# Kernel tuning notes

Hardware: AMD Instinct MI355X
Metric: run time of the kernel (lower is better)

## Reference

```python
import jax, jax.numpy as jnp
import numpy as np

MODEL_DIM = 256
NUM_HEAD = 8
HEAD_DIM = MODEL_DIM // NUM_HEAD  # 32
ROT_DIM_AXIS = int(0.5 * HEAD_DIM)  # 16 per axis, 32 total rotated channels
LN_EPS = 1e-5
MASK_BIAS = -1e9  # fp32 precision
SCALE = HEAD_DIM ** -0.5
INIT_RANGE = 0.02
N_LAYERS = 6


def _rotate_half(x):
    # interleaved pairs: (d r) with r=2 -> (-x2, x1) re-interleaved
    x = x.reshape(*x.shape[:-1], -1, 2)
    x1, x2 = x[..., 0], x[..., 1]
    return jnp.stack([-x2, x1], axis=-1).reshape(*x.shape[:-2], -1)


def _axial_freqs(seqlen):
    # RotaryEmbedding('lang' freqs) over t = linspace(-1, 1, seqlen)
    inv_freq = 1.0 / (10000.0 ** (jnp.arange(0, ROT_DIM_AXIS, 2, dtype=jnp.float32) / ROT_DIM_AXIS))
    t = jnp.linspace(-1.0, 1.0, seqlen, dtype=jnp.float32)
    f = jnp.repeat(t[:, None] * inv_freq[None, :], 2, axis=-1)  # (s, ROT_DIM_AXIS)
    fh = jnp.broadcast_to(f[:, None, :], (seqlen, seqlen, ROT_DIM_AXIS))
    fw = jnp.broadcast_to(f[None, :, :], (seqlen, seqlen, ROT_DIM_AXIS))
    return jnp.concatenate([fh, fw], axis=-1)  # (s, s, 2*ROT_DIM_AXIS)


def _apply_rotary(freqs, t):
    rot_dim = freqs.shape[-1]
    t_rot, t_pass = t[..., :rot_dim], t[..., rot_dim:]
    t_rot = t_rot * jnp.cos(freqs) + _rotate_half(t_rot) * jnp.sin(freqs)
    return jnp.concatenate([t_rot, t_pass], axis=-1)


def setup_inputs() -> dict:
    key = jax.random.key(0)
    k1, k2, k3, k4 = jax.random.split(key, 4)
    b, s = 2, 128
    pair_act = jax.random.normal(k1, (b, s, s, MODEL_DIM), dtype=jnp.float32)
    pair_mask = jax.random.randint(k2, (b, s, s), 0, 2).astype(bool)  # True = masked
    Wqkv = jax.random.normal(k3, (3 * MODEL_DIM, MODEL_DIM), dtype=jnp.float32) * INIT_RANGE
    Wout = jax.random.normal(k4, (MODEL_DIM, MODEL_DIM), dtype=jnp.float32) * (INIT_RANGE / np.sqrt(2 * N_LAYERS))
    ln_gamma = jnp.ones((MODEL_DIM,), dtype=jnp.float32)
    ln_beta = jnp.zeros((MODEL_DIM,), dtype=jnp.float32)
    return {"pair_act": pair_act, "pair_mask": pair_mask, "ln_gamma": ln_gamma,
            "ln_beta": ln_beta, "Wqkv": Wqkv, "Wout": Wout}


def reference(pair_act, pair_mask, ln_gamma, ln_beta, Wqkv, Wout):
    # orientation == 'per_row': no axis swap
    b, s = pair_act.shape[0], pair_act.shape[1]
    # LayerNorm over model_dim
    mu = jnp.mean(pair_act, axis=-1, keepdims=True)
    var = jnp.var(pair_act, axis=-1, keepdims=True)
    x = (pair_act - mu) * jax.lax.rsqrt(var + LN_EPS) * ln_gamma + ln_beta
    # QKV projection (no bias)
    qkv = jnp.einsum('bxyd,ed->bxye', x, Wqkv)  # (b, s, s, 3*MODEL_DIM)
    q, k, v = jnp.split(qkv, 3, axis=-1)
    # 2D axial rotary on first 2*ROT_DIM_AXIS channels of the feature dim
    freqs = _axial_freqs(s)  # (s, s, 32)
    q = _apply_rotary(freqs, q)
    k = _apply_rotary(freqs, k)
    # multihead attention per row (axis s1 independent)
    q = q.reshape(b, s, s, NUM_HEAD, HEAD_DIM)
    k = k.reshape(b, s, s, NUM_HEAD, HEAD_DIM)
    v = v.reshape(b, s, s, NUM_HEAD, HEAD_DIM)
    scores = jnp.einsum('bxqhd,bxkhd->bxhqk', q, k) * SCALE  # (b, s1, h, s2, s2)
    mask = pair_mask[:, :, None, None, :]  # (b, s1, 1, 1, s2)
    scores = jnp.where(mask, MASK_BIAS, scores)
    attn = jax.nn.softmax(scores, axis=-1)
    out = jnp.einsum('bxhqk,bxkhd->bxqhd', attn, v).reshape(b, s, s, MODEL_DIM)
    return jnp.einsum('bxyd,ed->bxye', out, Wout)
```

## Files before the change

### kernel.cpp

```cpp
#include <hip/hip_runtime.h>
#include <math.h>
#include <stdint.h>

typedef __attribute__((ext_vector_type(8))) short short8;
typedef __attribute__((ext_vector_type(4))) float floatx4;

#define LN_EPS 1e-5f
#define ATT_SCALE 0.17677669529663687f

__device__ __constant__ float INVF[8] = {
    1.0f, 0.31622776601683794f, 0.1f, 0.031622776601683794f,
    0.01f, 0.0031622776601683794f, 0.001f, 0.00031622776601683794f};

__device__ inline unsigned short f2bf(float f) {
    unsigned u = __float_as_uint(f);
    u += 0x7fffu + ((u >> 16) & 1u);
    return (unsigned short)(u >> 16);
}

__device__ inline void gl_lds16(const unsigned short* g, unsigned short* l) {
    __builtin_amdgcn_global_load_lds(
        (const __attribute__((address_space(1))) void*)(uintptr_t)g,
        (__attribute__((address_space(3))) void*)(uintptr_t)l, 16, 0, 0);
}

__device__ inline void stage_tile(const unsigned short* __restrict__ Wsrc,
                                  unsigned short* dst, int w, int lane) {
    #pragma unroll
    for (int i = 0; i < 4; ++i) {
        int rbase = i * 16 + w * 2;
        int row = rbase + (lane >> 5);
        int sl = lane & 31;
        int c = (sl & ~7) | ((sl & 7) ^ (row & 7));
        gl_lds16(Wsrc + (size_t)row * 256 + c * 8, dst + rbase * 256);
    }
}

#define VM0() asm volatile("s_waitcnt vmcnt(0)" ::: "memory")
#define LG0() asm volatile("s_waitcnt lgkmcnt(0)" ::: "memory")
#define SBAR()                                 \
    do {                                       \
        __builtin_amdgcn_s_barrier();          \
        __builtin_amdgcn_sched_barrier(0);     \
    } while (0)

__global__ __launch_bounds__(256)
void prep_w(const float* __restrict__ wq, const float* __restrict__ wo,
            unsigned short* __restrict__ bq, unsigned short* __restrict__ bo) {
    int g = blockIdx.x * 256 + threadIdx.x;
    const float* src;
    unsigned short* dst;
    if (g < 49152) { src = wq + (size_t)g * 4; dst = bq + (size_t)g * 4; }
    else { int h = g - 49152; src = wo + (size_t)h * 4; dst = bo + (size_t)h * 4; }
    float4 v = *(const float4*)src;
    uint2 o;
    o.x = (unsigned)f2bf(v.x) | ((unsigned)f2bf(v.y) << 16);
    o.y = (unsigned)f2bf(v.z) | ((unsigned)f2bf(v.w) << 16);
    *(uint2*)dst = o;
}

__global__ __launch_bounds__(512, 2)
void fused_kernel(const float* __restrict__ pair_act, const int* __restrict__ mask,
                  const float* __restrict__ gamma, const float* __restrict__ beta,
                  const unsigned short* __restrict__ Wqkv,
                  const unsigned short* __restrict__ Wout,
                  float* __restrict__ out) {
    __shared__ __align__(16) unsigned short S16[2][16384];
    __shared__ __align__(16) unsigned short Ks[2][128 * 40];
    __shared__ __align__(16) unsigned short Vt[2][32 * 136];
    __shared__ __align__(16) unsigned short Qall[8 * 1280];

    int bx = blockIdx.x;
    int tid = threadIdx.x;
    int w = tid >> 6, lane = tid & 63, qd = lane >> 4, lo = lane & 15;
    unsigned short* Qscr = Qall + w * 1280;

    float tX = -1.0f + (2.0f / 127.0f) * (float)(bx & 127);

    stage_tile(Wqkv, &S16[1][0], w, lane);

    float msel[8];
    #pragma unroll
    for (int nt = 0; nt < 8; ++nt)
        msel[nt] = mask[bx * 128 + nt * 16 + lo] ? 0.0f : 1.0f;

    short8 a_frag[8];
    {
        int rl = tid >> 2, q0 = tid & 3;
        const float* src = pair_act + ((size_t)(bx * 128 + rl)) * 256 + q0 * 4;
        float4 v[16];
        float s = 0.f;
        #pragma unroll
        for (int u = 0; u < 16; ++u) {
            v[u] = *(const float4*)(src + u * 16);
            s += v[u].x + v[u].y + v[u].z + v[u].w;
        }
        s += __shfl_xor(s, 1);
        s += __shfl_xor(s, 2);
        float mean = s * (1.0f / 256.0f);
        float sq = 0.f;
        #pragma unroll
        for (int u = 0; u < 16; ++u) {
            float d0 = v[u].x - mean, d1 = v[u].y - mean;
            float d2 = v[u].z - mean, d3 = v[u].w - mean;
            sq += d0 * d0 + d1 * d1 + d2 * d2 + d3 * d3;
        }
        sq += __shfl_xor(sq, 1);
        sq += __shfl_xor(sq, 2);
        float rs = rsqrtf(sq * (1.0f / 256.0f) + LN_EPS);

        int rw = 16 * w + lo;
        #pragma unroll
        for (int p = 0; p < 2; ++p) {
            #pragma unroll
            for (int ul = 0; ul < 8; ++ul) {
                int u = p * 8 + ul;
                float4 g4 = *(const float4*)(gamma + q0 * 4 + u * 16);
                float4 b4 = *(const float4*)(beta + q0 * 4 + u * 16);
                unsigned e0 = f2bf((v[u].x - mean) * rs * g4.x + b4.x);
                unsigned e1 = f2bf((v[u].y - mean) * rs * g4.y + b4.y);
                unsigned e2 = f2bf((v[u].z - mean) * rs * g4.z + b4.z);
                unsigned e3 = f2bf((v[u].w - mean) * rs * g4.w + b4.w);
                int cw = 2 * ul + (q0 >> 1);
                int ss = (cw & ~7) | ((cw & 7) ^ (rl & 7));
                uint2 pk;
                pk.x = e0 | (e1 << 16);
                pk.y = e2 | (e3 << 16);
                *(uint2*)&S16[0][rl * 128 + ss * 8 + (q0 & 1) * 4] = pk;
            }
            __syncthreads();
            #pragma unroll
            for (int cp = 0; cp < 4; ++cp) {
                int ci = cp * 4 + qd;
                int ss = (ci & ~7) | ((ci & 7) ^ (rw & 7));
                a_frag[p * 4 + cp] = *(const short8*)&S16[0][rw * 128 + ss * 8];
            }
            __syncthreads();
        }
    }

    unsigned q_pk[4][4][2], k_pk[4][4][2], v_pk[4][4][2];
    #pragma unroll
    for (int t = 0; t < 12; ++t) {
        VM0();
        SBAR();
        const unsigned short* nsrc =
            (t < 11) ? (Wqkv + (size_t)(t + 1) * 64 * 256) : Wout;
        stage_tile(nsrc, &S16[t & 1][0], w, lane);

        const unsigned short* Sb = &S16[(t + 1) & 1][0];
        floatx4 acc[4];
        #pragma unroll
        for (int tq = 0; tq < 4; ++tq) acc[tq] = (floatx4){0.f, 0.f, 0.f, 0.f};
        #pragma unroll
        for (int cc = 0; cc < 8; ++cc) {
            #pragma unroll
            for (int tq = 0; tq < 4; ++tq) {
                int rw2 = tq * 16 + lo;
                int ci = cc * 4 + qd;
                int ss = (ci & ~7) | ((ci & 7) ^ (rw2 & 7));
                short8 bf = *(const short8*)&Sb[rw2 * 256 + ss * 8];
                acc[tq] = __builtin_amdgcn_mfma_f32_16x16x32_bf16(
                    a_frag[cc], bf, acc[tq], 0, 0, 0);
            }
        }
        if (t == 0 || t == 4) {
            #pragma unroll
            for (int tc = 0; tc < 2; ++tc) {
                int pi = (tc * 16 + lo) >> 1;
                float invf = INVF[pi & 7];
                float sgn = (lo & 1) ? 1.0f : -1.0f;
                #pragma unroll
                for (int r = 0; r < 4; ++r) {
                    int y = 16 * w + qd * 4 + r;
                    float tp = (pi < 8) ? tX
                                        : (-1.0f + (2.0f / 127.0f) * (float)y);
                    float sn, cs;
                    __sincosf(tp * invf, &sn, &cs);
                    float vv = acc[tc][r];
                    float pv = __shfl_xor(vv, 1);
                    acc[tc][r] = vv * cs + sgn * pv * sn;
                }
            }
        }
        int part = t >> 2, hc = t & 3;
        #pragma unroll
        for (int tq = 0; tq < 4; ++tq) {
            unsigned p0 = (unsigned)f2bf(acc[tq][0]) |
                          ((unsigned)f2bf(acc[tq][1]) << 16);
            unsigned p1 = (unsigned)f2bf(acc[tq][2]) |
                          ((unsigned)f2bf(acc[tq][3]) << 16);
            if (part == 0) { q_pk[hc][tq][0] = p0; q_pk[hc][tq][1] = p1; }
            else if (part == 1) { k_pk[hc][tq][0] = p0; k_pk[hc][tq][1] = p1; }
            else { v_pk[hc][tq][0] = p0; v_pk[hc][tq][1] = p1; }
        }
    }

    float m2[8][4];
    #pragma unroll
    for (int nt = 0; nt < 8; ++nt)
        #pragma unroll
        for (int r = 0; r < 4; ++r)
            m2[nt][r] = __shfl(msel[nt], qd * 4 + r);

    {
        #pragma unroll
        for (int tt = 0; tt < 2; ++tt) {
            int tC = tt;
            int d = tt * 16 + lo;
            #pragma unroll
            for (int r = 0; r < 4; ++r) {
                unsigned kv = (k_pk[0][tC][r >> 1] >> ((r & 1) * 16)) & 0xffffu;
                Ks[0][(16 * w + qd * 4 + r) * 40 + d] = (unsigned short)kv;
            }
            uint2 pv;
            pv.x = v_pk[0][tC][0];
            pv.y = v_pk[0][tC][1];
            *(uint2*)&Vt[0][d * 136 + 16 * w + qd * 4] = pv;
        }
    }
    LG0();
    SBAR();
    stage_tile(Wout + (size_t)64 * 256, &S16[0][0], w, lane);

    #pragma unroll
    for (int tt = 0; tt < 2; ++tt)
        #pragma unroll
        for (int r = 0; r < 4; ++r) {
            unsigned qv = (q_pk[0][tt][r >> 1] >> ((r & 1) * 16)) & 0xffffu;
            Qscr[(qd * 4 + r) * 40 + tt * 16 + lo] = (unsigned short)qv;
        }

    short8 of[8];
    #pragma unroll
    for (int h = 0; h < 8; ++h) {
        if (h < 7) {
            int g = h + 1, hcg = g >> 1, tg0 = (g & 1) * 2, kb = g & 1;
            #pragma unroll
            for (int tt = 0; tt < 2; ++tt) {
                int tC = tg0 + tt;
                int d = tt * 16 + lo;
                #pragma unroll
                for (int r = 0; r < 4; ++r) {
                    unsigned kv =
                        (k_pk[hcg][tC][r >> 1] >> ((r & 1) * 16)) & 0xffffu;
                    Ks[kb][(16 * w + qd * 4 + r) * 40 + d] = (unsigned short)kv;
                }
                uint2 pv;
                pv.x = v_pk[hcg][tC][0];
                pv.y = v_pk[hcg][tC][1];
                *(uint2*)&Vt[kb][d * 136 + 16 * w + qd * 4] = pv;
            }
        }
        {
            int cb = h & 1;
            short8 aq = *(const short8*)&Qscr[(h & 1) * 640 + lo * 40 + qd * 8];
            if (h < 7) {
                int hn = h + 1, hch = hn >> 1;
                #pragma unroll
                for (int tt = 0; tt < 2; ++tt) {
                    int tC = (hn & 1) * 2 + tt;
                    #pragma unroll
                    for (int r = 0; r < 4; ++r) {
                        unsigned qv =
                            (q_pk[hch][tC][r >> 1] >> ((r & 1) * 16)) & 0xffffu;
                        Qscr[(hn & 1) * 640 + (qd * 4 + r) * 40 + tt * 16 + lo] =
                            (unsigned short)qv;
                    }
                }
            }
            int idx1 = (qd & 1) * 32 + lo;
            int idx2 = idx1 + 16;
            int sel = qd >> 1;
            float lsum = 0.f;
            floatx4 o2[2];
            o2[0] = (floatx4){0.f, 0.f, 0.f, 0.f};
            o2[1] = (floatx4){0.f, 0.f, 0.f, 0.f};
            #pragma unroll
            for (int c2 = 0; c2 < 4; ++c2) {
                short8 bk0 =
                    *(const short8*)&Ks[cb][((2 * c2) * 16 + lo) * 40 + qd * 8];
                short8 bk1 =
                    *(const short8*)&Ks[cb][((2 * c2 + 1) * 16 + lo) * 40 + qd * 8];
                floatx4 s0 = (floatx4){0.f, 0.f, 0.f, 0.f};
                floatx4 s1 = (floatx4){0.f, 0.f, 0.f, 0.f};
                s0 = __builtin_amdgcn_mfma_f32_16x16x32_bf16(bk0, aq, s0, 0, 0, 0);
                s1 = __builtin_amdgcn_mfma_f32_16x16x32_bf16(bk1, aq, s1, 0, 0, 0);
                float eA[4], eB[4];
                #pragma unroll
                for (int r = 0; r < 4; ++r) {
                    eA[r] = __expf(s0[r] * ATT_SCALE) * m2[2 * c2][r];
                    eB[r] = __expf(s1[r] * ATT_SCALE) * m2[2 * c2 + 1][r];
                    lsum += eA[r] + eB[r];
                }
                unsigned P0d0 = (unsigned)f2bf(eA[0]) | ((unsigned)f2bf(eA[1]) << 16);
                unsigned P0d1 = (unsigned)f2bf(eA[2]) | ((unsigned)f2bf(eA[3]) << 16);
                unsigned P1d0 = (unsigned)f2bf(eB[0]) | ((unsigned)f2bf(eB[1]) << 16);
                unsigned P1d1 = (unsigned)f2bf(eB[2]) | ((unsigned)f2bf(eB[3]) << 16);
                unsigned t10 = (unsigned)__shfl((int)P0d0, idx1);
                unsigned t11 = (unsigned)__shfl((int)P0d1, idx1);
                unsigned t12 = (unsigned)__shfl((int)P1d0, idx1);
                unsigned t13 = (unsigned)__shfl((int)P1d1, idx1);
                unsigned t20 = (unsigned)__shfl((int)P0d0, idx2);
                unsigned t21 = (unsigned)__shfl((int)P0d1, idx2);
                unsigned t22 = (unsigned)__shfl((int)P1d0, idx2);
                unsigned t23 = (unsigned)__shfl((int)P1d1, idx2);
                union { unsigned u[4]; short8 s8; } pa;
                pa.u[0] = sel ? t12 : t10;
                pa.u[1] = sel ? t13 : t11;
                pa.u[2] = sel ? t22 : t20;
                pa.u[3] = sel ? t23 : t21;
                #pragma unroll
                for (int n = 0; n < 2; ++n) {
                    short8 vb = *(const short8*)&Vt[cb][(n * 16 + lo) * 136 +
                                                        c2 * 32 + qd * 8];
                    o2[n] = __builtin_amdgcn_mfma_f32_16x16x32_bf16(pa.s8, vb,
                                                                    o2[n], 0, 0, 0);
                }
            }
            lsum += __shfl_xor(lsum, 16);
            lsum += __shfl_xor(lsum, 32);
            float invs = 1.0f / lsum;
            float inv_q[4];
            #pragma unroll
            for (int r = 0; r < 4; ++r) inv_q[r] = __shfl(invs, qd * 4 + r);
            #pragma unroll
            for (int n = 0; n < 2; ++n)
                #pragma unroll
                for (int r = 0; r < 4; ++r)
                    Qscr[(h & 1) * 640 + (qd * 4 + r) * 40 + n * 16 + lo] =
                        f2bf(o2[n][r] * inv_q[r]);
            of[h] = *(const short8*)&Qscr[(h & 1) * 640 + lo * 40 + qd * 8];
        }
        LG0();
        if (h == 7) VM0();
        SBAR();
    }

    #pragma unroll
    for (int nc = 0; nc < 4; ++nc) {
        if (nc) {
            VM0();
            SBAR();
            if (nc < 3)
                stage_tile(Wout + (size_t)(nc + 1) * 64 * 256,
                           &S16[nc & 1][0], w, lane);
        }
        const unsigned short* Sb = &S16[(nc + 1) & 1][0];
        floatx4 acc[4];
        #pragma unroll
        for (int tq = 0; tq < 4; ++tq) acc[tq] = (floatx4){0.f, 0.f, 0.f, 0.f};
        #pragma unroll
        for (int cc = 0; cc < 8; ++cc) {
            #pragma unroll
            for (int tq = 0; tq < 4; ++tq) {
                int rw2 = tq * 16 + lo;
                int ci = cc * 4 + qd;
                int ss = (ci & ~7) | ((ci & 7) ^ (rw2 & 7));
                short8 bf = *(const short8*)&Sb[rw2 * 256 + ss * 8];
                acc[tq] = __builtin_amdgcn_mfma_f32_16x16x32_bf16(
                    of[cc], bf, acc[tq], 0, 0, 0);
            }
        }
        #pragma unroll
        for (int tq = 0; tq < 4; ++tq)
            #pragma unroll
            for (int r = 0; r < 4; ++r)
                out[(size_t)(bx * 128 + 16 * w + qd * 4 + r) * 256 + nc * 64 +
                    tq * 16 + lo] = acc[tq][r];
    }
}

extern "C" void kernel_launch(void* const* d_in, const int* in_sizes, int n_in,
                              void* d_out, int out_size, void* d_ws, size_t ws_size,
                              hipStream_t stream) {
    const float* pair_act = (const float*)d_in[0];
    const int* pair_mask = (const int*)d_in[1];
    const float* ln_gamma = (const float*)d_in[2];
    const float* ln_beta = (const float*)d_in[3];
    const float* Wqkv = (const float*)d_in[4];
    const float* Wout = (const float*)d_in[5];
    float* out = (float*)d_out;

    char* ws = (char*)d_ws;
    unsigned short* wqkv_bf = (unsigned short*)ws;
    unsigned short* wout_bf = (unsigned short*)(ws + 393216);

    prep_w<<<256, 256, 0, stream>>>(Wqkv, Wout, wqkv_bf, wout_bf);
    fused_kernel<<<256, 512, 0, stream>>>(pair_act, pair_mask, ln_gamma, ln_beta,
                                          wqkv_bf, wout_bf, out);
}
```

Baseline: 140.2 us.

## Split waves into 2x4 row/column groups, processing two heads concurrently

Work is redistributed so each wave owns 32 rows and half of each 64-column weight tile (2x2 MFMA blocks) instead of 16 rows and the full tile. This halves B-fragment LDS reads per MFMA in the projections. Attention now runs two heads at once, one per column group, with K/V double-buffered per group, and each wave handles 32 query rows. Attention output is exchanged through a swizzled LDS buffer before the output projection. The cost is more registers (doubled A fragments and q/k/v packs), extra barriers per head pair, and reuse of the S16 staging buffer.

```diff
diff --git a/kernel.cpp b/kernel.cpp
--- a/kernel.cpp
+++ b/kernel.cpp
@@ -68,12 +68,14 @@
     __shared__ __align__(16) unsigned short S16[2][16384];
     __shared__ __align__(16) unsigned short Ks[2][128 * 40];
     __shared__ __align__(16) unsigned short Vt[2][32 * 136];
-    __shared__ __align__(16) unsigned short Qall[8 * 1280];
+    __shared__ __align__(16) unsigned short Qall[8][2560];
 
     int bx = blockIdx.x;
     int tid = threadIdx.x;
     int w = tid >> 6, lane = tid & 63, qd = lane >> 4, lo = lane & 15;
-    unsigned short* Qscr = Qall + w * 1280;
+    int cg = w >> 2, rg = w & 3;
+    unsigned short* Qscr = Qall[w];
+    unsigned short* Oex = &S16[0][0];
 
     float tX = -1.0f + (2.0f / 127.0f) * (float)(bx & 127);
 
@@ -84,7 +86,7 @@
     for (int nt = 0; nt < 8; ++nt)
         msel[nt] = mask[bx * 128 + nt * 16 + lo] ? 0.0f : 1.0f;
 
-    short8 a_frag[8];
+    short8 a_frag2[2][8];
     {
         int rl = tid >> 2, q0 = tid & 3;
         const float* src = pair_act + ((size_t)(bx * 128 + rl)) * 256 + q0 * 4;
@@ -107,9 +109,8 @@
         }
         sq += __shfl_xor(sq, 1);
         sq += __shfl_xor(sq, 2);
-        float rs = rsqrtf(sq * (1.0f / 256.0f) + LN_EPS);
-
-        int rw = 16 * w + lo;
+        float rs_ = rsqrtf(sq * (1.0f / 256.0f) + LN_EPS);
+
         #pragma unroll
         for (int p = 0; p < 2; ++p) {
             #pragma unroll
@@ -117,10 +118,10 @@
                 int u = p * 8 + ul;
                 float4 g4 = *(const float4*)(gamma + q0 * 4 + u * 16);
                 float4 b4 = *(const float4*)(beta + q0 * 4 + u * 16);
-                unsigned e0 = f2bf((v[u].x - mean) * rs * g4.x + b4.x);
-                unsigned e1 = f2bf((v[u].y - mean) * rs * g4.y + b4.y);
-                unsigned e2 = f2bf((v[u].z - mean) * rs * g4.z + b4.z);
-                unsigned e3 = f2bf((v[u].w - mean) * rs * g4.w + b4.w);
+                unsigned e0 = f2bf((v[u].x - mean) * rs_ * g4.x + b4.x);
+                unsigned e1 = f2bf((v[u].y - mean) * rs_ * g4.y + b4.y);
+                unsigned e2 = f2bf((v[u].z - mean) * rs_ * g4.z + b4.z);
+                unsigned e3 = f2bf((v[u].w - mean) * rs_ * g4.w + b4.w);
                 int cw = 2 * ul + (q0 >> 1);
                 int ss = (cw & ~7) | ((cw & 7) ^ (rl & 7));
                 uint2 pk;
@@ -130,70 +131,85 @@
             }
             __syncthreads();
             #pragma unroll
-            for (int cp = 0; cp < 4; ++cp) {
-                int ci = cp * 4 + qd;
-                int ss = (ci & ~7) | ((ci & 7) ^ (rw & 7));
-                a_frag[p * 4 + cp] = *(const short8*)&S16[0][rw * 128 + ss * 8];
+            for (int rs = 0; rs < 2; ++rs) {
+                int rw = 32 * rg + rs * 16 + lo;
+                #pragma unroll
+                for (int cp = 0; cp < 4; ++cp) {
+                    int ci = cp * 4 + qd;
+                    int ss = (ci & ~7) | ((ci & 7) ^ (rw & 7));
+                    a_frag2[rs][p * 4 + cp] =
+                        *(const short8*)&S16[0][rw * 128 + ss * 8];
+                }
             }
             __syncthreads();
         }
     }
 
-    unsigned q_pk[4][4][2], k_pk[4][4][2], v_pk[4][4][2];
+    unsigned q_pk[4][2][2][2], k_pk[4][2][2][2], v_pk[4][2][2][2];
     #pragma unroll
     for (int t = 0; t < 12; ++t) {
         VM0();
         SBAR();
-        const unsigned short* nsrc =
-            (t < 11) ? (Wqkv + (size_t)(t + 1) * 64 * 256) : Wout;
-        stage_tile(nsrc, &S16[t & 1][0], w, lane);
+        if (t < 11)
+            stage_tile(Wqkv + (size_t)(t + 1) * 64 * 256, &S16[t & 1][0], w, lane);
 
         const unsigned short* Sb = &S16[(t + 1) & 1][0];
-        floatx4 acc[4];
-        #pragma unroll
-        for (int tq = 0; tq < 4; ++tq) acc[tq] = (floatx4){0.f, 0.f, 0.f, 0.f};
+        floatx4 acc[2][2];
+        #pragma unroll
+        for (int rs = 0; rs < 2; ++rs)
+            #pragma unroll
+            for (int tq = 0; tq < 2; ++tq)
+                acc[rs][tq] = (floatx4){0.f, 0.f, 0.f, 0.f};
         #pragma unroll
         for (int cc = 0; cc < 8; ++cc) {
-            #pragma unroll
-            for (int tq = 0; tq < 4; ++tq) {
-                int rw2 = tq * 16 + lo;
-                int ci = cc * 4 + qd;
-                int ss = (ci & ~7) | ((ci & 7) ^ (rw2 & 7));
-                short8 bf = *(const short8*)&Sb[rw2 * 256 + ss * 8];
-                acc[tq] = __builtin_amdgcn_mfma_f32_16x16x32_bf16(
-                    a_frag[cc], bf, acc[tq], 0, 0, 0);
+            int ci = cc * 4 + qd;
+            int ss = (ci & ~7) | ((ci & 7) ^ (lo & 7));
+            short8 bf0 = *(const short8*)&Sb[(cg * 32 + lo) * 256 + ss * 8];
+            short8 bf1 = *(const short8*)&Sb[(cg * 32 + 16 + lo) * 256 + ss * 8];
+            acc[0][0] = __builtin_amdgcn_mfma_f32_16x16x32_bf16(
+                a_frag2[0][cc], bf0, acc[0][0], 0, 0, 0);
+            acc[0][1] = __builtin_amdgcn_mfma_f32_16x16x32_bf16(
+                a_frag2[0][cc], bf1, acc[0][1], 0, 0, 0);
+            acc[1][0] = __builtin_amdgcn_mfma_f32_16x16x32_bf16(
+                a_frag2[1][cc], bf0, acc[1][0], 0, 0, 0);
+            acc[1][1] = __builtin_amdgcn_mfma_f32_16x16x32_bf16(
+                a_frag2[1][cc], bf1, acc[1][1], 0, 0, 0);
+        }
+        if ((t == 0 || t == 4) && cg == 0) {
+            #pragma unroll
+            for (int rs = 0; rs < 2; ++rs)
+                #pragma unroll
+                for (int tq = 0; tq < 2; ++tq) {
+                    int pi = (tq * 16 + lo) >> 1;
+                    float invf = INVF[pi & 7];
+                    float sgn = (lo & 1) ? 1.0f : -1.0f;
+                    #pragma unroll
+                    for (int r = 0; r < 4; ++r) {
+                        int y = 32 * rg + rs * 16 + qd * 4 + r;
+                        float tp = (pi < 8)
+                                       ? tX
+                                       : (-1.0f + (2.0f / 127.0f) * (float)y);
+                        float sn, cs;
+                        __sincosf(tp * invf, &sn, &cs);
+                        float vv = acc[rs][tq][r];
+                        float pv = __shfl_xor(vv, 1);
+                        acc[rs][tq][r] = vv * cs + sgn * pv * sn;
+                    }
+                }
+        }
+        int part = t >> 2, hc = t & 3;
+        #pragma unroll
+        for (int rs = 0; rs < 2; ++rs)
+            #pragma unroll
+            for (int tq = 0; tq < 2; ++tq) {
+                unsigned p0 = (unsigned)f2bf(acc[rs][tq][0]) |
+                              ((unsigned)f2bf(acc[rs][tq][1]) << 16);
+                unsigned p1 = (unsigned)f2bf(acc[rs][tq][2]) |
+                              ((unsigned)f2bf(acc[rs][tq][3]) << 16);
+                if (part == 0) { q_pk[hc][rs][tq][0] = p0; q_pk[hc][rs][tq][1] = p1; }
+                else if (part == 1) { k_pk[hc][rs][tq][0] = p0; k_pk[hc][rs][tq][1] = p1; }
+                else { v_pk[hc][rs][tq][0] = p0; v_pk[hc][rs][tq][1] = p1; }
             }
-        }
-        if (t == 0 || t == 4) {
-            #pragma unroll
-            for (int tc = 0; tc < 2; ++tc) {
-                int pi = (tc * 16 + lo) >> 1;
-                float invf = INVF[pi & 7];
-                float sgn = (lo & 1) ? 1.0f : -1.0f;
-                #pragma unroll
-                for (int r = 0; r < 4; ++r) {
-                    int y = 16 * w + qd * 4 + r;
-                    float tp = (pi < 8) ? tX
-                                        : (-1.0f + (2.0f / 127.0f) * (float)y);
-                    float sn, cs;
-                    __sincosf(tp * invf, &sn, &cs);
-                    float vv = acc[tc][r];
-                    float pv = __shfl_xor(vv, 1);
-                    acc[tc][r] = vv * cs + sgn * pv * sn;
-                }
-            }
-        }
-        int part = t >> 2, hc = t & 3;
-        #pragma unroll
-        for (int tq = 0; tq < 4; ++tq) {
-            unsigned p0 = (unsigned)f2bf(acc[tq][0]) |
-                          ((unsigned)f2bf(acc[tq][1]) << 16);
-            unsigned p1 = (unsigned)f2bf(acc[tq][2]) |
-                          ((unsigned)f2bf(acc[tq][3]) << 16);
-            if (part == 0) { q_pk[hc][tq][0] = p0; q_pk[hc][tq][1] = p1; }
-            else if (part == 1) { k_pk[hc][tq][0] = p0; k_pk[hc][tq][1] = p1; }
-            else { v_pk[hc][tq][0] = p0; v_pk[hc][tq][1] = p1; }
-        }
     }
 
     float m2[8][4];
@@ -203,95 +219,87 @@
         for (int r = 0; r < 4; ++r)
             m2[nt][r] = __shfl(msel[nt], qd * 4 + r);
 
-    {
-        #pragma unroll
-        for (int tt = 0; tt < 2; ++tt) {
-            int tC = tt;
-            int d = tt * 16 + lo;
-            #pragma unroll
-            for (int r = 0; r < 4; ++r) {
-                unsigned kv = (k_pk[0][tC][r >> 1] >> ((r & 1) * 16)) & 0xffffu;
-                Ks[0][(16 * w + qd * 4 + r) * 40 + d] = (unsigned short)kv;
+    auto stage_kv = [&](int hcn) {
+        #pragma unroll
+        for (int rs = 0; rs < 2; ++rs)
+            #pragma unroll
+            for (int tt = 0; tt < 2; ++tt) {
+                int d = tt * 16 + lo;
+                #pragma unroll
+                for (int r = 0; r < 4; ++r) {
+                    unsigned kv =
+                        (k_pk[hcn][rs][tt][r >> 1] >> ((r & 1) * 16)) & 0xffffu;
+                    Ks[cg][(32 * rg + rs * 16 + qd * 4 + r) * 40 + d] =
+                        (unsigned short)kv;
+                }
+                uint2 pv;
+                pv.x = v_pk[hcn][rs][tt][0];
+                pv.y = v_pk[hcn][rs][tt][1];
+                *(uint2*)&Vt[cg][d * 136 + 32 * rg + rs * 16 + qd * 4] = pv;
             }
-            uint2 pv;
-            pv.x = v_pk[0][tC][0];
-            pv.y = v_pk[0][tC][1];
-            *(uint2*)&Vt[0][d * 136 + 16 * w + qd * 4] = pv;
-        }
-    }
+    };
+    auto write_q = [&](int hcn) {
+        unsigned short* qs = Qscr + (hcn & 1) * 1280;
+        #pragma unroll
+        for (int rs = 0; rs < 2; ++rs)
+            #pragma unroll
+            for (int tt = 0; tt < 2; ++tt)
+                #pragma unroll
+                for (int r = 0; r < 4; ++r) {
+                    unsigned qv =
+                        (q_pk[hcn][rs][tt][r >> 1] >> ((r & 1) * 16)) & 0xffffu;
+                    qs[(rs * 16 + qd * 4 + r) * 40 + tt * 16 + lo] =
+                        (unsigned short)qv;
+                }
+    };
+
+    stage_kv(0);
     LG0();
     SBAR();
-    stage_tile(Wout + (size_t)64 * 256, &S16[0][0], w, lane);
-
-    #pragma unroll
-    for (int tt = 0; tt < 2; ++tt)
-        #pragma unroll
-        for (int r = 0; r < 4; ++r) {
-            unsigned qv = (q_pk[0][tt][r >> 1] >> ((r & 1) * 16)) & 0xffffu;
-            Qscr[(qd * 4 + r) * 40 + tt * 16 + lo] = (unsigned short)qv;
-        }
-
-    short8 of[8];
-    #pragma unroll
-    for (int h = 0; h < 8; ++h) {
-        if (h < 7) {
-            int g = h + 1, hcg = g >> 1, tg0 = (g & 1) * 2, kb = g & 1;
-            #pragma unroll
-            for (int tt = 0; tt < 2; ++tt) {
-                int tC = tg0 + tt;
-                int d = tt * 16 + lo;
-                #pragma unroll
-                for (int r = 0; r < 4; ++r) {
-                    unsigned kv =
-                        (k_pk[hcg][tC][r >> 1] >> ((r & 1) * 16)) & 0xffffu;
-                    Ks[kb][(16 * w + qd * 4 + r) * 40 + d] = (unsigned short)kv;
-                }
-                uint2 pv;
-                pv.x = v_pk[hcg][tC][0];
-                pv.y = v_pk[hcg][tC][1];
-                *(uint2*)&Vt[kb][d * 136 + 16 * w + qd * 4] = pv;
-            }
-        }
-        {
-            int cb = h & 1;
-            short8 aq = *(const short8*)&Qscr[(h & 1) * 640 + lo * 40 + qd * 8];
-            if (h < 7) {
-                int hn = h + 1, hch = hn >> 1;
-                #pragma unroll
-                for (int tt = 0; tt < 2; ++tt) {
-                    int tC = (hn & 1) * 2 + tt;
-                    #pragma unroll
-                    for (int r = 0; r < 4; ++r) {
-                        unsigned qv =
-                            (q_pk[hch][tC][r >> 1] >> ((r & 1) * 16)) & 0xffffu;
-                        Qscr[(hn & 1) * 640 + (qd * 4 + r) * 40 + tt * 16 + lo] =
-                            (unsigned short)qv;
-                    }
-                }
-            }
-            int idx1 = (qd & 1) * 32 + lo;
-            int idx2 = idx1 + 16;
-            int sel = qd >> 1;
-            float lsum = 0.f;
-            floatx4 o2[2];
-            o2[0] = (floatx4){0.f, 0.f, 0.f, 0.f};
-            o2[1] = (floatx4){0.f, 0.f, 0.f, 0.f};
-            #pragma unroll
-            for (int c2 = 0; c2 < 4; ++c2) {
-                short8 bk0 =
-                    *(const short8*)&Ks[cb][((2 * c2) * 16 + lo) * 40 + qd * 8];
-                short8 bk1 =
-                    *(const short8*)&Ks[cb][((2 * c2 + 1) * 16 + lo) * 40 + qd * 8];
+    write_q(0);
+
+    #pragma unroll
+    for (int hc = 0; hc < 4; ++hc) {
+        int h = hc * 2 + cg;
+        const unsigned short* qs = Qscr + (hc & 1) * 1280;
+        short8 aq[2];
+        aq[0] = *(const short8*)&qs[lo * 40 + qd * 8];
+        aq[1] = *(const short8*)&qs[(16 + lo) * 40 + qd * 8];
+        if (hc < 3) write_q(hc + 1);
+
+        int idx1 = (qd & 1) * 32 + lo;
+        int idx2 = idx1 + 16;
+        int sel = qd >> 1;
+        float lsum[2] = {0.f, 0.f};
+        floatx4 o2[2][2];
+        #pragma unroll
+        for (int rs = 0; rs < 2; ++rs)
+            #pragma unroll
+            for (int n = 0; n < 2; ++n)
+                o2[rs][n] = (floatx4){0.f, 0.f, 0.f, 0.f};
+
+        #pragma unroll
+        for (int c2 = 0; c2 < 4; ++c2) {
+            short8 bk0 =
+                *(const short8*)&Ks[cg][((2 * c2) * 16 + lo) * 40 + qd * 8];
+            short8 bk1 =
+                *(const short8*)&Ks[cg][((2 * c2 + 1) * 16 + lo) * 40 + qd * 8];
+            short8 vb0 =
+                *(const short8*)&Vt[cg][lo * 136 + c2 * 32 + qd * 8];
+            short8 vb1 =
+                *(const short8*)&Vt[cg][(16 + lo) * 136 + c2 * 32 + qd * 8];
+            #pragma unroll
+            for (int rs = 0; rs < 2; ++rs) {
                 floatx4 s0 = (floatx4){0.f, 0.f, 0.f, 0.f};
                 floatx4 s1 = (floatx4){0.f, 0.f, 0.f, 0.f};
-                s0 = __builtin_amdgcn_mfma_f32_16x16x32_bf16(bk0, aq, s0, 0, 0, 0);
-                s1 = __builtin_amdgcn_mfma_f32_16x16x32_bf16(bk1, aq, s1, 0, 0, 0);
+                s0 = __builtin_amdgcn_mfma_f32_16x16x32_bf16(bk0, aq[rs], s0, 0, 0, 0);
+                s1 = __builtin_amdgcn_mfma_f32_16x16x32_bf16(bk1, aq[rs], s1, 0, 0, 0);
                 float eA[4], eB[4];
                 #pragma unroll
                 for (int r = 0; r < 4; ++r) {
                     eA[r] = __expf(s0[r] * ATT_SCALE) * m2[2 * c2][r];
                     eB[r] = __expf(s1[r] * ATT_SCALE) * m2[2 * c2 + 1][r];
-                    lsum += eA[r] + eB[r];
+                    lsum[rs] += eA[r] + eB[r];
                 }
                 unsigned P0d0 = (unsigned)f2bf(eA[0]) | ((unsigned)f2bf(eA[1]) << 16);
                 unsigned P0d1 = (unsigned)f2bf(eA[2]) | ((unsigned)f2bf(eA[3]) << 16);
@@ -310,64 +318,95 @@
                 pa.u[1] = sel ? t13 : t11;
                 pa.u[2] = sel ? t22 : t20;
                 pa.u[3] = sel ? t23 : t21;
-                #pragma unroll
-                for (int n = 0; n < 2; ++n) {
-                    short8 vb = *(const short8*)&Vt[cb][(n * 16 + lo) * 136 +
-                                                        c2 * 32 + qd * 8];
-                    o2[n] = __builtin_amdgcn_mfma_f32_16x16x32_bf16(pa.s8, vb,
-                                                                    o2[n], 0, 0, 0);
-                }
+                o2[rs][0] = __builtin_amdgcn_mfma_f32_16x16x32_bf16(
+                    pa.s8, vb0, o2[rs][0], 0, 0, 0);
+                o2[rs][1] = __builtin_amdgcn_mfma_f32_16x16x32_bf16(
+                    pa.s8, vb1, o2[rs][1], 0, 0, 0);
             }
-            lsum += __shfl_xor(lsum, 16);
-            lsum += __shfl_xor(lsum, 32);
-            float invs = 1.0f / lsum;
-            float inv_q[4];
-            #pragma unroll
-            for (int r = 0; r < 4; ++r) inv_q[r] = __shfl(invs, qd * 4 + r);
+        }
+        float inv_q[2][4];
+        #pragma unroll
+        for (int rs = 0; rs < 2; ++rs) {
+            float vv = lsum[rs];
+            vv += __shfl_xor(vv, 16);
+            vv += __shfl_xor(vv, 32);
+            float invs = 1.0f / vv;
+            #pragma unroll
+            for (int r = 0; r < 4; ++r)
+                inv_q[rs][r] = __shfl(invs, qd * 4 + r);
+        }
+        #pragma unroll
+        for (int rs = 0; rs < 2; ++rs)
             #pragma unroll
             for (int n = 0; n < 2; ++n)
                 #pragma unroll
+                for (int r = 0; r < 4; ++r) {
+                    int row = 32 * rg + rs * 16 + qd * 4 + r;
+                    int col = h * 32 + n * 16 + lo;
+                    Oex[row * 256 + (col ^ ((row & 7) << 3))] =
+                        f2bf(o2[rs][n][r] * inv_q[rs][r]);
+                }
+
+        LG0();
+        SBAR();
+        if (hc < 3) {
+            stage_kv(hc + 1);
+            LG0();
+            SBAR();
+        }
+    }
+
+    short8 of2[2][8];
+    #pragma unroll
+    for (int rs = 0; rs < 2; ++rs) {
+        int row = 32 * rg + rs * 16 + lo;
+        #pragma unroll
+        for (int cc = 0; cc < 8; ++cc) {
+            int cb2 = (cc * 32 + qd * 8) ^ ((row & 7) << 3);
+            of2[rs][cc] = *(const short8*)&Oex[row * 256 + cb2];
+        }
+    }
+    LG0();
+    SBAR();
+    stage_tile(Wout, &S16[1][0], w, lane);
+
+    #pragma unroll
+    for (int nc = 0; nc < 4; ++nc) {
+        VM0();
+        SBAR();
+        if (nc < 3)
+            stage_tile(Wout + (size_t)(nc + 1) * 64 * 256, &S16[nc & 1][0], w,
+                       lane);
+        const unsigned short* Sb = &S16[(nc + 1) & 1][0];
+        floatx4 acc[2][2];
+        #pragma unroll
+        for (int rs = 0; rs < 2; ++rs)
+            #pragma unroll
+            for (int tq = 0; tq < 2; ++tq)
+                acc[rs][tq] = (floatx4){0.f, 0.f, 0.f, 0.f};
+        #pragma unroll
+        for (int cc = 0; cc < 8; ++cc) {
+            int ci = cc * 4 + qd;
+            int ss = (ci & ~7) | ((ci & 7) ^ (lo & 7));
+            short8 bf0 = *(const short8*)&Sb[(cg * 32 + lo) * 256 + ss * 8];
+            short8 bf1 = *(const short8*)&Sb[(cg * 32 + 16 + lo) * 256 + ss * 8];
+            acc[0][0] = __builtin_amdgcn_mfma_f32_16x16x32_bf16(
+                of2[0][cc], bf0, acc[0][0], 0, 0, 0);
+            acc[0][1] = __builtin_amdgcn_mfma_f32_16x16x32_bf16(
+                of2[0][cc], bf1, acc[0][1], 0, 0, 0);
+            acc[1][0] = __builtin_amdgcn_mfma_f32_16x16x32_bf16(
+                of2[1][cc], bf0, acc[1][0], 0, 0, 0);
+            acc[1][1] = __builtin_amdgcn_mfma_f32_16x16x32_bf16(
+                of2[1][cc], bf1, acc[1][1], 0, 0, 0);
+        }
+        #pragma unroll
+        for (int rs = 0; rs < 2; ++rs)
+            #pragma unroll
+            for (int tq = 0; tq < 2; ++tq)
+                #pragma unroll
                 for (int r = 0; r < 4; ++r)
-                    Qscr[(h & 1) * 640 + (qd * 4 + r) * 40 + n * 16 + lo] =
-                        f2bf(o2[n][r] * inv_q[r]);
-            of[h] = *(const short8*)&Qscr[(h & 1) * 640 + lo * 40 + qd * 8];
-        }
-        LG0();
-        if (h == 7) VM0();
-        SBAR();
-    }
-
-    #pragma unroll
-    for (int nc = 0; nc < 4; ++nc) {
-        if (nc) {
-            VM0();
-            SBAR();
-            if (nc < 3)
-                stage_tile(Wout + (size_t)(nc + 1) * 64 * 256,
-                           &S16[nc & 1][0], w, lane);
-        }
-        const unsigned short* Sb = &S16[(nc + 1) & 1][0];
-        floatx4 acc[4];
-        #pragma unroll
-        for (int tq = 0; tq < 4; ++tq) acc[tq] = (floatx4){0.f, 0.f, 0.f, 0.f};
-        #pragma unroll
-        for (int cc = 0; cc < 8; ++cc) {
-            #pragma unroll
-            for (int tq = 0; tq < 4; ++tq) {
-                int rw2 = tq * 16 + lo;
-                int ci = cc * 4 + qd;
-                int ss = (ci & ~7) | ((ci & 7) ^ (rw2 & 7));
-                short8 bf = *(const short8*)&Sb[rw2 * 256 + ss * 8];
-                acc[tq] = __builtin_amdgcn_mfma_f32_16x16x32_bf16(
-                    of[cc], bf, acc[tq], 0, 0, 0);
-            }
-        }
-        #pragma unroll
-        for (int tq = 0; tq < 4; ++tq)
-            #pragma unroll
-            for (int r = 0; r < 4; ++r)
-                out[(size_t)(bx * 128 + 16 * w + qd * 4 + r) * 256 + nc * 64 +
-                    tq * 16 + lo] = acc[tq][r];
+                    out[(size_t)(bx * 128 + 32 * rg + rs * 16 + qd * 4 + r) * 256 +
+                        nc * 64 + cg * 32 + tq * 16 + lo] = acc[rs][tq][r];
     }
 }
 
```

Result: slower. 150.6 us (+7.5%).
